# Optimization experiments

Measured on AMD Instinct MI355X. Metric: run time of the kernel, lower is better.

The kernel has to match this reference:

```python
import jax, jax.numpy as jnp
import numpy as np

N, K, D = 8192, 4096, 256


def setup_inputs() -> dict:
    key = jax.random.key(0)
    kx, kc, kw = jax.random.split(key, 3)
    x = jax.random.normal(kx, (N, D), dtype=jnp.float32)
    centers = jax.random.normal(kc, (K, D), dtype=jnp.float32)
    w = jax.random.normal(kw, (K,), dtype=jnp.float32)
    # bandwidth chosen so exp(-sigma * d2) stays in a healthy range for
    # Gaussian data where E[||x-c||^2] ~= 2*D
    sigma = jnp.asarray(1.0 / (2.0 * D), dtype=jnp.float32)
    return {"x": x, "centers": centers, "w": w, "sigma": sigma}


def reference(x, centers, w, sigma):
    # phi[n,k] = exp(-sigma * ||x_n - c_k||^2), computed via the GEMM
    x2 = jnp.sum(x * x, axis=-1, keepdims=True)          # [N,1]
    c2 = jnp.sum(centers * centers, axis=-1)             # [K]
    d2 = x2 + c2 - 2.0 * jnp.einsum('nd,kd->nk', x, centers)  # [N,K]
    d2 = jnp.maximum(d2, 0.0)  # clamp tiny negative round-off
    phi = jnp.exp(-sigma * d2)                           # [N,K]
    # (w * phi).sum(1) == phi @ w
    return jnp.einsum('nk,k->n', phi, w)                 # [N]
```

## Files before the change

### kernel.cpp

```cpp
#include <hip/hip_runtime.h>

#define NROWS 8192
#define NCENT 4096
#define DIM   256

#define AS1 __attribute__((address_space(1)))
#define AS3 __attribute__((address_space(3)))

typedef short bf16x8 __attribute__((ext_vector_type(8)));
typedef float f32x4  __attribute__((ext_vector_type(4)));

__device__ inline unsigned short f2bf(float f) {
    unsigned u = __float_as_uint(f);
    return (unsigned short)((u + 0x7fffu + ((u >> 16) & 1u)) >> 16);
}

__global__ __launch_bounds__(256) void prep_kernel(const float* __restrict__ x,
                                                   const float* __restrict__ c,
                                                   float* __restrict__ norms,
                                                   unsigned short* __restrict__ xbf,
                                                   unsigned short* __restrict__ cbf,
                                                   float* __restrict__ out) {
    const int t = threadIdx.x, lane = t & 63;
    if (blockIdx.x < NROWS / 256) out[blockIdx.x * 256 + t] = 0.0f;
    const int wbase = (blockIdx.x * 4 + (t >> 6)) * 4;
    #pragma unroll
    for (int rr = 0; rr < 4; ++rr) {
        const int gw = wbase + rr;
        const float* src;
        unsigned short* dst;
        if (gw < NROWS) { src = x + (size_t)gw * DIM;           dst = xbf + (size_t)gw * DIM; }
        else            { src = c + (size_t)(gw - NROWS) * DIM; dst = cbf + (size_t)(gw - NROWS) * DIM; }
        float4 v = ((const float4*)src)[lane];
        ushort4 b;
        b.x = f2bf(v.x); b.y = f2bf(v.y); b.z = f2bf(v.z); b.w = f2bf(v.w);
        ((ushort4*)dst)[lane] = b;
        float s = v.x * v.x + v.y * v.y + v.z * v.z + v.w * v.w;
        #pragma unroll
        for (int m = 32; m; m >>= 1) s += __shfl_xor(s, m);
        if (lane == 0) norms[gw] = s;
    }
}

#define BUFH (128 * 32)

__global__ __launch_bounds__(256) void rbf_mfma(const unsigned short* __restrict__ xbf,
                                                const unsigned short* __restrict__ cbf,
                                                const float* __restrict__ w,
                                                const float* __restrict__ sigp,
                                                const float* __restrict__ norms,
                                                float* __restrict__ out) {
    __shared__ __align__(16) short As[2 * BUFH];
    __shared__ __align__(16) short Bs[2 * BUFH];

    const int t    = threadIdx.x;
    const int wave = t >> 6, lane = t & 63;
    const int m0   = blockIdx.y * 128;
    const int n0   = blockIdx.x * 128;
    const int wy   = wave >> 1, wx = wave & 1;
    const int lr   = lane & 15;
    const int g    = lane >> 4;

    const int r_in = lane >> 2;
    const int c_l  = (lane & 3) ^ ((r_in >> 1) & 3);
    const unsigned short* ga0 = xbf + (size_t)(m0 + 32 * wave + r_in) * DIM + c_l * 8;
    const unsigned short* ga1 = ga0 + 16 * DIM;
    const unsigned short* gb0 = cbf + (size_t)(n0 + 32 * wave + r_in) * DIM + c_l * 8;
    const unsigned short* gb1 = gb0 + 16 * DIM;
    short* la0 = As + (32 * wave) * 32;
    short* lb0 = Bs + (32 * wave) * 32;

#define STAGE(buf, kk) do {                                                                  \
        const int ko_ = (kk) * 32;                                                           \
        __builtin_amdgcn_global_load_lds((const AS1 void*)(ga0 + ko_),                       \
                                         (AS3 void*)(la0 + (buf) * BUFH), 16, 0, 0);         \
        __builtin_amdgcn_global_load_lds((const AS1 void*)(ga1 + ko_),                       \
                                         (AS3 void*)(la0 + (buf) * BUFH + 16 * 32), 16, 0, 0);\
        __builtin_amdgcn_global_load_lds((const AS1 void*)(gb0 + ko_),                       \
                                         (AS3 void*)(lb0 + (buf) * BUFH), 16, 0, 0);         \
        __builtin_amdgcn_global_load_lds((const AS1 void*)(gb1 + ko_),                       \
                                         (AS3 void*)(lb0 + (buf) * BUFH + 16 * 32), 16, 0, 0);\
    } while (0)

    int aoff[4], boff[4];
    #pragma unroll
    for (int i = 0; i < 4; ++i) {
        int r = 64 * wy + 16 * i + lr;
        aoff[i] = r * 32 + ((g ^ ((r >> 1) & 3)) * 8);
    }
    #pragma unroll
    for (int j = 0; j < 4; ++j) {
        int r = 64 * wx + 16 * j + lr;
        boff[j] = r * 32 + ((g ^ ((r >> 1) & 3)) * 8);
    }

    f32x4 acc[4][4];
    #pragma unroll
    for (int i = 0; i < 4; ++i)
        #pragma unroll
        for (int j = 0; j < 4; ++j) acc[i][j] = f32x4{0, 0, 0, 0};

    STAGE(0, 0);
    __syncthreads();

    #pragma unroll
    for (int kk = 0; kk < DIM / 32; ++kk) {
        const int cur = kk & 1;
        if (kk < DIM / 32 - 1) STAGE(cur ^ 1, kk + 1);

        const short* Ab = As + cur * BUFH;
        const short* Bb = Bs + cur * BUFH;
        bf16x8 a[4], b[4];
        #pragma unroll
        for (int i = 0; i < 4; ++i) a[i] = *(const bf16x8*)(Ab + aoff[i]);
        #pragma unroll
        for (int j = 0; j < 4; ++j) b[j] = *(const bf16x8*)(Bb + boff[j]);
        #pragma unroll
        for (int i = 0; i < 4; ++i)
            #pragma unroll
            for (int j = 0; j < 4; ++j)
                acc[i][j] = __builtin_amdgcn_mfma_f32_16x16x32_bf16(a[i], b[j], acc[i][j], 0, 0, 0);

        __syncthreads();
    }
#undef STAGE

    const float sigma = sigp[0];
    const float* x2 = norms;
    const float* c2 = norms + NROWS;

    float c2v[4], wv[4];
    #pragma unroll
    for (int j = 0; j < 4; ++j) {
        int n = n0 + 64 * wx + 16 * j + lr;
        c2v[j] = c2[n];
        wv[j]  = w[n];
    }

    #pragma unroll
    for (int i = 0; i < 4; ++i) {
        const int mbase = m0 + 64 * wy + 16 * i + 4 * g;
        float4 x2v = *(const float4*)(x2 + mbase);
        float rs[4] = {0.f, 0.f, 0.f, 0.f};
        #pragma unroll
        for (int j = 0; j < 4; ++j) {
            #pragma unroll
            for (int r = 0; r < 4; ++r) {
                float x2r = (r == 0) ? x2v.x : (r == 1) ? x2v.y : (r == 2) ? x2v.z : x2v.w;
                float d2 = x2r + c2v[j] - 2.0f * acc[i][j][r];
                d2 = fmaxf(d2, 0.0f);
                rs[r] += wv[j] * __expf(-sigma * d2);
            }
        }
        #pragma unroll
        for (int r = 0; r < 4; ++r) {
            rs[r] += __shfl_xor(rs[r], 1);
            rs[r] += __shfl_xor(rs[r], 2);
            rs[r] += __shfl_xor(rs[r], 4);
            rs[r] += __shfl_xor(rs[r], 8);
        }
        if (lr == 0) {
            #pragma unroll
            for (int r = 0; r < 4; ++r) atomicAdd(&out[mbase + r], rs[r]);
        }
    }
}

__global__ __launch_bounds__(256) void norms_kernel(const float* __restrict__ x,
                                                    const float* __restrict__ c,
                                                    float* __restrict__ ws) {
    int t = threadIdx.x, lane = t & 63;
    int gw = blockIdx.x * 4 + (t >> 6);
    const float* src;
    float* dst;
    if (gw < NROWS) { src = x + (size_t)gw * DIM;           dst = ws + gw; }
    else            { src = c + (size_t)(gw - NROWS) * DIM; dst = ws + gw; }
    float4 v = ((const float4*)src)[lane];
    float s = v.x * v.x + v.y * v.y + v.z * v.z + v.w * v.w;
    #pragma unroll
    for (int m = 32; m; m >>= 1) s += __shfl_xor(s, m);
    if (lane == 0) *dst = s;
}

__global__ __launch_bounds__(256) void rbf_kernel(const float* __restrict__ x,
                                                  const float* __restrict__ cent,
                                                  const float* __restrict__ w,
                                                  const float* __restrict__ sigp,
                                                  const float* __restrict__ norms,
                                                  float* __restrict__ out) {
    __shared__ __align__(16) short xs[64 * 32];
    __shared__ __align__(16) short cs[64 * 32];
    const int t = threadIdx.x;
    const int m0 = blockIdx.y * 64, n0 = blockIdx.x * 64;
    const int srow = t >> 2, seg = t & 3;
    const int pchunk = seg ^ ((srow >> 1) & 3);
    const int sidx = srow * 32 + pchunk * 8;
    const float* xg = x    + (size_t)(m0 + srow) * DIM + seg * 8;
    const float* cg = cent + (size_t)(n0 + srow) * DIM + seg * 8;
    const int lane = t & 63, wave = t >> 6;
    const int lr = lane & 15, lg = lane >> 4;
    const int arow = 16 * wave + lr;
    const int aidx = arow * 32 + ((lg ^ ((arow >> 1) & 3)) * 8);
    f32x4 acc[4] = {f32x4{0,0,0,0}, f32x4{0,0,0,0}, f32x4{0,0,0,0}, f32x4{0,0,0,0}};
    for (int k0 = 0; k0 < DIM; k0 += 32) {
        float4 f0 = *(const float4*)(xg + k0);
        float4 f1 = *(const float4*)(xg + k0 + 4);
        float4 g0 = *(const float4*)(cg + k0);
        float4 g1 = *(const float4*)(cg + k0 + 4);
        __syncthreads();
        union { unsigned short s[8]; int4 v; } ux, uc;
        ux.s[0]=f2bf(f0.x); ux.s[1]=f2bf(f0.y); ux.s[2]=f2bf(f0.z); ux.s[3]=f2bf(f0.w);
        ux.s[4]=f2bf(f1.x); ux.s[5]=f2bf(f1.y); ux.s[6]=f2bf(f1.z); ux.s[7]=f2bf(f1.w);
        uc.s[0]=f2bf(g0.x); uc.s[1]=f2bf(g0.y); uc.s[2]=f2bf(g0.z); uc.s[3]=f2bf(g0.w);
        uc.s[4]=f2bf(g1.x); uc.s[5]=f2bf(g1.y); uc.s[6]=f2bf(g1.z); uc.s[7]=f2bf(g1.w);
        *(int4*)(xs + sidx) = ux.v;
        *(int4*)(cs + sidx) = uc.v;
        __syncthreads();
        bf16x8 a = *(const bf16x8*)(xs + aidx);
        #pragma unroll
        for (int bt = 0; bt < 4; ++bt) {
            const int brow = 16 * bt + lr;
            bf16x8 b = *(const bf16x8*)(cs + brow * 32 + ((lg ^ ((brow >> 1) & 3)) * 8));
            acc[bt] = __builtin_amdgcn_mfma_f32_16x16x32_bf16(a, b, acc[bt], 0, 0, 0);
        }
    }
    const float sigma = sigp[0];
    const float* x2 = norms;
    const float* c2 = norms + NROWS;
    const int rbase = m0 + 16 * wave + lg * 4;
    float x2v[4];
    #pragma unroll
    for (int r = 0; r < 4; ++r) x2v[r] = x2[rbase + r];
    float rs[4] = {0.f, 0.f, 0.f, 0.f};
    #pragma unroll
    for (int bt = 0; bt < 4; ++bt) {
        const int col = n0 + 16 * bt + lr;
        const float c2v = c2[col];
        const float wvv = w[col];
        #pragma unroll
        for (int r = 0; r < 4; ++r) {
            float d2 = x2v[r] + c2v - 2.0f * acc[bt][r];
            d2 = fmaxf(d2, 0.0f);
            rs[r] += wvv * __expf(-sigma * d2);
        }
    }
    #pragma unroll
    for (int r = 0; r < 4; ++r) {
        rs[r] += __shfl_xor(rs[r], 1);
        rs[r] += __shfl_xor(rs[r], 2);
        rs[r] += __shfl_xor(rs[r], 4);
        rs[r] += __shfl_xor(rs[r], 8);
    }
    if (lr == 0) {
        #pragma unroll
        for (int r = 0; r < 4; ++r) atomicAdd(&out[rbase + r], rs[r]);
    }
}

extern "C" void kernel_launch(void* const* d_in, const int* in_sizes, int n_in,
                              void* d_out, int out_size, void* d_ws, size_t ws_size,
                              hipStream_t stream) {
    const float* x    = (const float*)d_in[0];
    const float* cent = (const float*)d_in[1];
    const float* w    = (const float*)d_in[2];
    const float* sig  = (const float*)d_in[3];
    float* out = (float*)d_out;

    const size_t norms_elems = NROWS + NCENT;
    const size_t xbf_off  = norms_elems * sizeof(float);
    const size_t cbf_off  = xbf_off + (size_t)NROWS * DIM * sizeof(unsigned short);
    const size_t ws_need  = cbf_off + (size_t)NCENT * DIM * sizeof(unsigned short);

    if (ws_size >= ws_need) {
        float* norms = (float*)d_ws;
        unsigned short* xbf = (unsigned short*)((char*)d_ws + xbf_off);
        unsigned short* cbf = (unsigned short*)((char*)d_ws + cbf_off);
        prep_kernel<<<(NROWS + NCENT) / 16, 256, 0, stream>>>(x, cent, norms, xbf, cbf, out);
        rbf_mfma<<<dim3(NCENT / 128, NROWS / 128), 256, 0, stream>>>(xbf, cbf, w, sig, norms, out);
    } else {
        float* norms = (float*)d_ws;
        hipMemsetAsync(d_out, 0, (size_t)out_size * sizeof(float), stream);
        norms_kernel<<<(NROWS + NCENT) / 4, 256, 0, stream>>>(x, cent, norms);
        rbf_kernel<<<dim3(NCENT / 64, NROWS / 64), 256, 0, stream>>>(x, cent, w, sig, norms, out);
    }
}
```

Before: 103.1 us.

## Fuse bf16 conversion and norm computation into the MFMA RBF kernel

Removes the separate prep kernel. The main tile kernel now loads fp32 x and centers directly, converts them to bf16 in registers, stores them to LDS and accumulates the row norms on the fly. The norms are reduced through LDS for the epilogue, and the output is zeroed with a memset. This drops one launch and the bf16 workspace round trip. In exchange each tile reads fp32 (twice the bytes, re-read by many blocks), does redundant conversions, and gives up the async global_load_lds path for synchronous register staging.

```diff
diff --git a/kernel.cpp b/kernel.cpp
--- a/kernel.cpp
+++ b/kernel.cpp
@@ -3,9 +3,6 @@
 #define NROWS 8192
 #define NCENT 4096
 #define DIM   256
-
-#define AS1 __attribute__((address_space(1)))
-#define AS3 __attribute__((address_space(3)))
 
 typedef short bf16x8 __attribute__((ext_vector_type(8)));
 typedef float f32x4  __attribute__((ext_vector_type(4)));
@@ -15,43 +12,17 @@
     return (unsigned short)((u + 0x7fffu + ((u >> 16) & 1u)) >> 16);
 }
 
-__global__ __launch_bounds__(256) void prep_kernel(const float* __restrict__ x,
-                                                   const float* __restrict__ c,
-                                                   float* __restrict__ norms,
-                                                   unsigned short* __restrict__ xbf,
-                                                   unsigned short* __restrict__ cbf,
-                                                   float* __restrict__ out) {
-    const int t = threadIdx.x, lane = t & 63;
-    if (blockIdx.x < NROWS / 256) out[blockIdx.x * 256 + t] = 0.0f;
-    const int wbase = (blockIdx.x * 4 + (t >> 6)) * 4;
-    #pragma unroll
-    for (int rr = 0; rr < 4; ++rr) {
-        const int gw = wbase + rr;
-        const float* src;
-        unsigned short* dst;
-        if (gw < NROWS) { src = x + (size_t)gw * DIM;           dst = xbf + (size_t)gw * DIM; }
-        else            { src = c + (size_t)(gw - NROWS) * DIM; dst = cbf + (size_t)(gw - NROWS) * DIM; }
-        float4 v = ((const float4*)src)[lane];
-        ushort4 b;
-        b.x = f2bf(v.x); b.y = f2bf(v.y); b.z = f2bf(v.z); b.w = f2bf(v.w);
-        ((ushort4*)dst)[lane] = b;
-        float s = v.x * v.x + v.y * v.y + v.z * v.z + v.w * v.w;
-        #pragma unroll
-        for (int m = 32; m; m >>= 1) s += __shfl_xor(s, m);
-        if (lane == 0) norms[gw] = s;
-    }
-}
-
 #define BUFH (128 * 32)
 
-__global__ __launch_bounds__(256) void rbf_mfma(const unsigned short* __restrict__ xbf,
-                                                const unsigned short* __restrict__ cbf,
-                                                const float* __restrict__ w,
-                                                const float* __restrict__ sigp,
-                                                const float* __restrict__ norms,
-                                                float* __restrict__ out) {
+__global__ __launch_bounds__(256) void rbf_fused(const float* __restrict__ x,
+                                                 const float* __restrict__ cent,
+                                                 const float* __restrict__ w,
+                                                 const float* __restrict__ sigp,
+                                                 float* __restrict__ out) {
     __shared__ __align__(16) short As[2 * BUFH];
     __shared__ __align__(16) short Bs[2 * BUFH];
+    __shared__ float nA[128];
+    __shared__ float nB[128];
 
     const int t    = threadIdx.x;
     const int wave = t >> 6, lane = t & 63;
@@ -62,24 +33,45 @@
     const int g    = lane >> 4;
 
     const int r_in = lane >> 2;
-    const int c_l  = (lane & 3) ^ ((r_in >> 1) & 3);
-    const unsigned short* ga0 = xbf + (size_t)(m0 + 32 * wave + r_in) * DIM + c_l * 8;
-    const unsigned short* ga1 = ga0 + 16 * DIM;
-    const unsigned short* gb0 = cbf + (size_t)(n0 + 32 * wave + r_in) * DIM + c_l * 8;
-    const unsigned short* gb1 = gb0 + 16 * DIM;
-    short* la0 = As + (32 * wave) * 32;
-    short* lb0 = Bs + (32 * wave) * 32;
+    const int s4   = lane & 3;
+    const int c_l  = s4 ^ ((r_in >> 1) & 3);
+    const float* gax[2];
+    const float* gbx[2];
+    #pragma unroll
+    for (int h = 0; h < 2; ++h) {
+        gax[h] = x    + (size_t)(m0 + 32 * wave + 16 * h + r_in) * DIM + c_l * 8;
+        gbx[h] = cent + (size_t)(n0 + 32 * wave + 16 * h + r_in) * DIM + c_l * 8;
+    }
+    short* la[2];
+    short* lb[2];
+    #pragma unroll
+    for (int h = 0; h < 2; ++h) {
+        la[h] = As + (32 * wave + 16 * h + r_in) * 32 + s4 * 8;
+        lb[h] = Bs + (32 * wave + 16 * h + r_in) * 32 + s4 * 8;
+    }
+
+    float nrmA[2] = {0.f, 0.f}, nrmB[2] = {0.f, 0.f};
 
 #define STAGE(buf, kk) do {                                                                  \
         const int ko_ = (kk) * 32;                                                           \
-        __builtin_amdgcn_global_load_lds((const AS1 void*)(ga0 + ko_),                       \
-                                         (AS3 void*)(la0 + (buf) * BUFH), 16, 0, 0);         \
-        __builtin_amdgcn_global_load_lds((const AS1 void*)(ga1 + ko_),                       \
-                                         (AS3 void*)(la0 + (buf) * BUFH + 16 * 32), 16, 0, 0);\
-        __builtin_amdgcn_global_load_lds((const AS1 void*)(gb0 + ko_),                       \
-                                         (AS3 void*)(lb0 + (buf) * BUFH), 16, 0, 0);         \
-        __builtin_amdgcn_global_load_lds((const AS1 void*)(gb1 + ko_),                       \
-                                         (AS3 void*)(lb0 + (buf) * BUFH + 16 * 32), 16, 0, 0);\
+        _Pragma("unroll")                                                                    \
+        for (int h = 0; h < 2; ++h) {                                                        \
+            f32x4 a0 = *(const f32x4*)(gax[h] + ko_);                                        \
+            f32x4 a1 = *(const f32x4*)(gax[h] + ko_ + 4);                                    \
+            f32x4 b0 = *(const f32x4*)(gbx[h] + ko_);                                        \
+            f32x4 b1 = *(const f32x4*)(gbx[h] + ko_ + 4);                                    \
+            nrmA[h] += a0[0]*a0[0]+a0[1]*a0[1]+a0[2]*a0[2]+a0[3]*a0[3]                       \
+                     + a1[0]*a1[0]+a1[1]*a1[1]+a1[2]*a1[2]+a1[3]*a1[3];                      \
+            nrmB[h] += b0[0]*b0[0]+b0[1]*b0[1]+b0[2]*b0[2]+b0[3]*b0[3]                       \
+                     + b1[0]*b1[0]+b1[1]*b1[1]+b1[2]*b1[2]+b1[3]*b1[3];                      \
+            union { unsigned short s[8]; int4 v; } ua, ub;                                   \
+            ua.s[0]=f2bf(a0[0]); ua.s[1]=f2bf(a0[1]); ua.s[2]=f2bf(a0[2]); ua.s[3]=f2bf(a0[3]);\
+            ua.s[4]=f2bf(a1[0]); ua.s[5]=f2bf(a1[1]); ua.s[6]=f2bf(a1[2]); ua.s[7]=f2bf(a1[3]);\
+            ub.s[0]=f2bf(b0[0]); ub.s[1]=f2bf(b0[1]); ub.s[2]=f2bf(b0[2]); ub.s[3]=f2bf(b0[3]);\
+            ub.s[4]=f2bf(b1[0]); ub.s[5]=f2bf(b1[1]); ub.s[6]=f2bf(b1[2]); ub.s[7]=f2bf(b1[3]);\
+            *(int4*)(la[h] + (buf) * BUFH) = ua.v;                                           \
+            *(int4*)(lb[h] + (buf) * BUFH) = ub.v;                                           \
+        }                                                                                    \
     } while (0)
 
     int aoff[4], boff[4];
@@ -125,29 +117,42 @@
     }
 #undef STAGE
 
+    #pragma unroll
+    for (int h = 0; h < 2; ++h) {
+        nrmA[h] += __shfl_xor(nrmA[h], 1);
+        nrmA[h] += __shfl_xor(nrmA[h], 2);
+        nrmB[h] += __shfl_xor(nrmB[h], 1);
+        nrmB[h] += __shfl_xor(nrmB[h], 2);
+        if (s4 == 0) {
+            nA[32 * wave + 16 * h + r_in] = nrmA[h];
+            nB[32 * wave + 16 * h + r_in] = nrmB[h];
+        }
+    }
+    __syncthreads();
+
     const float sigma = sigp[0];
-    const float* x2 = norms;
-    const float* c2 = norms + NROWS;
 
     float c2v[4], wv[4];
     #pragma unroll
     for (int j = 0; j < 4; ++j) {
-        int n = n0 + 64 * wx + 16 * j + lr;
-        c2v[j] = c2[n];
-        wv[j]  = w[n];
+        int nl = 64 * wx + 16 * j + lr;
+        c2v[j] = nB[nl];
+        wv[j]  = w[n0 + nl];
     }
 
     #pragma unroll
     for (int i = 0; i < 4; ++i) {
-        const int mbase = m0 + 64 * wy + 16 * i + 4 * g;
-        float4 x2v = *(const float4*)(x2 + mbase);
+        const int mloc  = 64 * wy + 16 * i + 4 * g;
+        const int mbase = m0 + mloc;
+        float x2v[4];
+        #pragma unroll
+        for (int r = 0; r < 4; ++r) x2v[r] = nA[mloc + r];
         float rs[4] = {0.f, 0.f, 0.f, 0.f};
         #pragma unroll
         for (int j = 0; j < 4; ++j) {
             #pragma unroll
             for (int r = 0; r < 4; ++r) {
-                float x2r = (r == 0) ? x2v.x : (r == 1) ? x2v.y : (r == 2) ? x2v.z : x2v.w;
-                float d2 = x2r + c2v[j] - 2.0f * acc[i][j][r];
+                float d2 = x2v[r] + c2v[j] - 2.0f * acc[i][j][r];
                 d2 = fmaxf(d2, 0.0f);
                 rs[r] += wv[j] * __expf(-sigma * d2);
             }
@@ -166,97 +171,6 @@
     }
 }
 
-__global__ __launch_bounds__(256) void norms_kernel(const float* __restrict__ x,
-                                                    const float* __restrict__ c,
-                                                    float* __restrict__ ws) {
-    int t = threadIdx.x, lane = t & 63;
-    int gw = blockIdx.x * 4 + (t >> 6);
-    const float* src;
-    float* dst;
-    if (gw < NROWS) { src = x + (size_t)gw * DIM;           dst = ws + gw; }
-    else            { src = c + (size_t)(gw - NROWS) * DIM; dst = ws + gw; }
-    float4 v = ((const float4*)src)[lane];
-    float s = v.x * v.x + v.y * v.y + v.z * v.z + v.w * v.w;
-    #pragma unroll
-    for (int m = 32; m; m >>= 1) s += __shfl_xor(s, m);
-    if (lane == 0) *dst = s;
-}
-
-__global__ __launch_bounds__(256) void rbf_kernel(const float* __restrict__ x,
-                                                  const float* __restrict__ cent,
-                                                  const float* __restrict__ w,
-                                                  const float* __restrict__ sigp,
-                                                  const float* __restrict__ norms,
-                                                  float* __restrict__ out) {
-    __shared__ __align__(16) short xs[64 * 32];
-    __shared__ __align__(16) short cs[64 * 32];
-    const int t = threadIdx.x;
-    const int m0 = blockIdx.y * 64, n0 = blockIdx.x * 64;
-    const int srow = t >> 2, seg = t & 3;
-    const int pchunk = seg ^ ((srow >> 1) & 3);
-    const int sidx = srow * 32 + pchunk * 8;
-    const float* xg = x    + (size_t)(m0 + srow) * DIM + seg * 8;
-    const float* cg = cent + (size_t)(n0 + srow) * DIM + seg * 8;
-    const int lane = t & 63, wave = t >> 6;
-    const int lr = lane & 15, lg = lane >> 4;
-    const int arow = 16 * wave + lr;
-    const int aidx = arow * 32 + ((lg ^ ((arow >> 1) & 3)) * 8);
-    f32x4 acc[4] = {f32x4{0,0,0,0}, f32x4{0,0,0,0}, f32x4{0,0,0,0}, f32x4{0,0,0,0}};
-    for (int k0 = 0; k0 < DIM; k0 += 32) {
-        float4 f0 = *(const float4*)(xg + k0);
-        float4 f1 = *(const float4*)(xg + k0 + 4);
-        float4 g0 = *(const float4*)(cg + k0);
-        float4 g1 = *(const float4*)(cg + k0 + 4);
-        __syncthreads();
-        union { unsigned short s[8]; int4 v; } ux, uc;
-        ux.s[0]=f2bf(f0.x); ux.s[1]=f2bf(f0.y); ux.s[2]=f2bf(f0.z); ux.s[3]=f2bf(f0.w);
-        ux.s[4]=f2bf(f1.x); ux.s[5]=f2bf(f1.y); ux.s[6]=f2bf(f1.z); ux.s[7]=f2bf(f1.w);
-        uc.s[0]=f2bf(g0.x); uc.s[1]=f2bf(g0.y); uc.s[2]=f2bf(g0.z); uc.s[3]=f2bf(g0.w);
-        uc.s[4]=f2bf(g1.x); uc.s[5]=f2bf(g1.y); uc.s[6]=f2bf(g1.z); uc.s[7]=f2bf(g1.w);
-        *(int4*)(xs + sidx) = ux.v;
-        *(int4*)(cs + sidx) = uc.v;
-        __syncthreads();
-        bf16x8 a = *(const bf16x8*)(xs + aidx);
-        #pragma unroll
-        for (int bt = 0; bt < 4; ++bt) {
-            const int brow = 16 * bt + lr;
-            bf16x8 b = *(const bf16x8*)(cs + brow * 32 + ((lg ^ ((brow >> 1) & 3)) * 8));
-            acc[bt] = __builtin_amdgcn_mfma_f32_16x16x32_bf16(a, b, acc[bt], 0, 0, 0);
-        }
-    }
-    const float sigma = sigp[0];
-    const float* x2 = norms;
-    const float* c2 = norms + NROWS;
-    const int rbase = m0 + 16 * wave + lg * 4;
-    float x2v[4];
-    #pragma unroll
-    for (int r = 0; r < 4; ++r) x2v[r] = x2[rbase + r];
-    float rs[4] = {0.f, 0.f, 0.f, 0.f};
-    #pragma unroll
-    for (int bt = 0; bt < 4; ++bt) {
-        const int col = n0 + 16 * bt + lr;
-        const float c2v = c2[col];
-        const float wvv = w[col];
-        #pragma unroll
-        for (int r = 0; r < 4; ++r) {
-            float d2 = x2v[r] + c2v - 2.0f * acc[bt][r];
-            d2 = fmaxf(d2, 0.0f);
-            rs[r] += wvv * __expf(-sigma * d2);
-        }
-    }
-    #pragma unroll
-    for (int r = 0; r < 4; ++r) {
-        rs[r] += __shfl_xor(rs[r], 1);
-        rs[r] += __shfl_xor(rs[r], 2);
-        rs[r] += __shfl_xor(rs[r], 4);
-        rs[r] += __shfl_xor(rs[r], 8);
-    }
-    if (lr == 0) {
-        #pragma unroll
-        for (int r = 0; r < 4; ++r) atomicAdd(&out[rbase + r], rs[r]);
-    }
-}
-
 extern "C" void kernel_launch(void* const* d_in, const int* in_sizes, int n_in,
                               void* d_out, int out_size, void* d_ws, size_t ws_size,
                               hipStream_t stream) {
@@ -266,21 +180,6 @@
     const float* sig  = (const float*)d_in[3];
     float* out = (float*)d_out;
 
-    const size_t norms_elems = NROWS + NCENT;
-    const size_t xbf_off  = norms_elems * sizeof(float);
-    const size_t cbf_off  = xbf_off + (size_t)NROWS * DIM * sizeof(unsigned short);
-    const size_t ws_need  = cbf_off + (size_t)NCENT * DIM * sizeof(unsigned short);
-
-    if (ws_size >= ws_need) {
-        float* norms = (float*)d_ws;
-        unsigned short* xbf = (unsigned short*)((char*)d_ws + xbf_off);
-        unsigned short* cbf = (unsigned short*)((char*)d_ws + cbf_off);
-        prep_kernel<<<(NROWS + NCENT) / 16, 256, 0, stream>>>(x, cent, norms, xbf, cbf, out);
-        rbf_mfma<<<dim3(NCENT / 128, NROWS / 128), 256, 0, stream>>>(xbf, cbf, w, sig, norms, out);
-    } else {
-        float* norms = (float*)d_ws;
-        hipMemsetAsync(d_out, 0, (size_t)out_size * sizeof(float), stream);
-        norms_kernel<<<(NROWS + NCENT) / 4, 256, 0, stream>>>(x, cent, norms);
-        rbf_kernel<<<dim3(NCENT / 64, NROWS / 64), 256, 0, stream>>>(x, cent, w, sig, norms, out);
-    }
+    hipMemsetAsync(d_out, 0, (size_t)out_size * sizeof(float), stream);
+    rbf_fused<<<dim3(NCENT / 128, NROWS / 128), 256, 0, stream>>>(x, cent, w, sig, out);
 }
```

Result: slower. 180.9 us (+75.5%).
